# Kernel tuning notes

Hardware: AMD Instinct MI355X
Metric: run time of the kernel (lower is better)

The kernel has to match this reference:

```python
import jax, jax.numpy as jnp
import numpy as np
import math

K = 20        # args.k  (global-branch neighbors)
KL = 20       # args.kl (local-branch neighbors)
EPS = 1e-5    # BatchNorm eps
SLOPE = 0.2   # LeakyReLU slope


def _knn(x, k, keep):
    # x: [B,C,N]; keep: [B,N] bool column mask. pd = -||xi - xj||^2.
    xx = jnp.sum(x * x, axis=1)                          # [B,N]
    inner = jnp.einsum('bci,bcj->bij', x, x)             # [B,N,N]
    pd = 2.0 * inner - xx[:, :, None] - xx[:, None, :]
    mn = jnp.min(pd, axis=-1)                            # per-row min
    # suppressed columns are set to the row min so topk never selects them
    pd = jnp.where(keep[:, None, :], pd, mn[:, :, None])
    return jax.lax.top_k(pd, k)[1]                       # [B,N,k]


def _gather(pts, idx):
    # pts: [B,N,C], idx: [B,N,k] -> [B,N,k,C]
    b = jnp.arange(pts.shape[0])[:, None, None]
    return pts[b, idx]


def _edge_feat(x, k, keep, smooth):
    # DGCNN edge features: concat(neighbor - center, center) -> [B,2C,N,k]
    idx = _knn(x, k, keep)
    xp = jnp.transpose(x, (0, 2, 1))                     # [B,N,C]
    if smooth:
        # GraphLayer: neighbors come from a topk-mean smoothed field
        knn_x = _gather(xp, idx)                         # [B,N,k,C]
        k2 = math.ceil(k * 2 / 3)
        top = jax.lax.top_k(jnp.transpose(knn_x, (0, 1, 3, 2)), k2)[0]
        src = jnp.mean(top, axis=-1)                     # [B,N,C]
    else:
        src = xp
    feat = _gather(src, idx)                             # [B,N,k,C]
    ctr = jnp.broadcast_to(xp[:, :, None, :], feat.shape)
    out = jnp.concatenate([feat - ctr, ctr], axis=-1)    # [B,N,k,2C]
    return jnp.transpose(out, (0, 3, 1, 2))


def _bn(y, axes):
    # BatchNorm (training-mode batch stats, gamma=1, beta=0 as at init)
    mu = jnp.mean(y, axis=axes, keepdims=True)
    var = jnp.var(y, axis=axes, keepdims=True)
    return (y - mu) * jax.lax.rsqrt(var + EPS)


def _conv_block(x, w, axes):
    # 1x1 conv (no bias) + BN + LeakyReLU
    ein = 'oc,bcnk->bonk' if x.ndim == 4 else 'oc,bcn->bon'
    return jax.nn.leaky_relu(_bn(jnp.einsum(ein, w, x), axes), SLOPE)


def _forward(x, local_idx, w1, w2, w3, w4, w5, w6, w7, w8, w9,
             l1w, l2w, l2b, l3w, l3b):
    keep_l = local_idx
    keep_g = jnp.logical_not(local_idx)
    ax4 = (0, 2, 3)
    # local (smoothed GraphLayer) branch, neighbors restricted to local points
    xl1 = _conv_block(_edge_feat(x,   KL, keep_l, True), w1, ax4).max(-1)
    xl2 = _conv_block(_edge_feat(xl1, KL, keep_l, True), w2, ax4).max(-1)
    xl3 = _conv_block(_edge_feat(xl2, KL, keep_l, True), w3, ax4).max(-1)
    xl4 = _conv_block(_edge_feat(xl3, KL, keep_l, True), w4, ax4).max(-1)
    x_local = jnp.concatenate([xl1, xl2, xl3, xl4], axis=1)  # [B,512,N]
    # global branch, neighbors restricted to non-local points
    xg1 = _conv_block(_edge_feat(x,   K, keep_g, False), w5, ax4).max(-1)
    xg2 = _conv_block(_edge_feat(xg1, K, keep_g, False), w6, ax4).max(-1)
    xg3 = _conv_block(_edge_feat(xg2, K, keep_g, False), w7, ax4).max(-1)
    xg4 = _conv_block(_edge_feat(xg3, K, keep_g, False), w8, ax4).max(-1)
    x_glob = jnp.concatenate([xg1, xg2, xg3, xg4], axis=1)   # [B,512,N]
    # per-point merge: local columns take the local-branch features
    h = jnp.where(local_idx[:, None, :], x_local, x_glob)
    h = _conv_block(h, w9, (0, 2))                            # [B,E,N]
    g = jnp.concatenate([h.max(-1), h.mean(-1)], axis=1)      # [B,2E]
    # head: linears + BN1d + LeakyReLU; dropout is identity (eval mode)
    g = jax.nn.leaky_relu(_bn(g @ l1w.T, (0,)), SLOPE)
    g = jax.nn.leaky_relu(_bn(g @ l2w.T + l2b, (0,)), SLOPE)
    return g @ l3w.T + l3b


def setup_inputs() -> dict:
    key = jax.random.key(0)
    ks = jax.random.split(key, 16)
    B, N, E, OUT = 4, 2048, 1024, 40

    def w(k, o, i):
        return jax.random.normal(k, (o, i), jnp.float32) / np.sqrt(i)

    return {
        'x': jax.random.normal(ks[0], (B, 3, N), jnp.float32),
        'local_idx': jax.random.bernoulli(ks[1], 0.5, (B, N)),
        'geod_dist': jax.random.normal(ks[2], (B, N), jnp.float32),
        'w1': w(ks[3], 64, 6),   'w2': w(ks[4], 64, 128),
        'w3': w(ks[5], 128, 128), 'w4': w(ks[6], 256, 256),
        'w5': w(ks[7], 64, 6),   'w6': w(ks[8], 64, 128),
        'w7': w(ks[9], 128, 128), 'w8': w(ks[10], 256, 256),
        'w9': w(ks[11], E, 512),
        'l1w': w(ks[12], 512, 2 * E),
        'l2w': w(ks[13], 256, 512),
        'l2b': jnp.zeros((256,), jnp.float32),
        'l3w': w(ks[14], OUT, 256),
        'l3b': jnp.zeros((OUT,), jnp.float32),
    }


def reference(x, local_idx, geod_dist, w1, w2, w3, w4, w5, w6, w7, w8, w9,
              l1w, l2w, l2b, l3w, l3b):
    del geod_dist  # accepted but unused in the original forward
    return _forward(x, local_idx, w1, w2, w3, w4, w5, w6, w7, w8, w9,
                    l1w, l2w, l2b, l3w, l3b)
```

## Files before the change

kernel.cpp:

```cpp
#include <hip/hip_runtime.h>
#include <hip/hip_bf16.h>
#include <cfloat>

#define BB 4
#define NN 2048
#define KNN 20
#define KTOP 14
#define EPSBN 1e-5f
#define SLOPE 0.2f

__global__ void k_xx3(const float* __restrict__ x, float* __restrict__ xx) {
  int t = blockIdx.x * 64 + threadIdx.x;
  int b = t >> 11, n = t & 2047;
  const float* xb = x + (long)b * (3L * NN) + n;
  float v0 = xb[0], v1 = xb[NN], v2 = xb[2 * NN];
  xx[t] = v0 * v0 + v1 * v1 + v2 * v2;
}

__device__ __forceinline__ void top1_tree(const float v[32], float& bv, int& bi) {
  float mv[16]; int mi[16];
#pragma unroll
  for (int s = 0; s < 16; ++s) {
    mi[s] = (v[2 * s] >= v[2 * s + 1]) ? 2 * s : 2 * s + 1;
    mv[s] = fmaxf(v[2 * s], v[2 * s + 1]);
  }
#pragma unroll
  for (int s = 0; s < 8; ++s) {
    mi[s] = (mv[2 * s] >= mv[2 * s + 1]) ? mi[2 * s] : mi[2 * s + 1];
    mv[s] = fmaxf(mv[2 * s], mv[2 * s + 1]);
  }
#pragma unroll
  for (int s = 0; s < 4; ++s) {
    mi[s] = (mv[2 * s] >= mv[2 * s + 1]) ? mi[2 * s] : mi[2 * s + 1];
    mv[s] = fmaxf(mv[2 * s], mv[2 * s + 1]);
  }
  int i01 = (mv[0] >= mv[1]) ? mi[0] : mi[1];
  float v01 = fmaxf(mv[0], mv[1]);
  int i23 = (mv[2] >= mv[3]) ? mi[2] : mi[3];
  float v23 = fmaxf(mv[2], mv[3]);
  bi = (v01 >= v23) ? i01 : i23;
  bv = fmaxf(v01, v23);
}

__device__ __forceinline__ void remove_slot(float v[32], int bi) {
#pragma unroll
  for (int s = 0; s < 32; ++s)
    if (s == bi) v[s] = -FLT_MAX;
}

__device__ __forceinline__ void sel_reg(const float* __restrict__ trow,
                                        const int* __restrict__ lrow,
                                        int keepv, int lane,
                                        int* __restrict__ orow) {
  int base = 4 * lane;
  float v[32];
#pragma unroll
  for (int q = 0; q < 8; ++q) {
    float4 lv = *(const float4*)(trow + 256 * q + base);
    int4 kv = *(const int4*)(lrow + 256 * q + base);
    v[4 * q + 0] = (((kv.x != 0) ? 1 : 0) == keepv) ? lv.x : -FLT_MAX;
    v[4 * q + 1] = (((kv.y != 0) ? 1 : 0) == keepv) ? lv.y : -FLT_MAX;
    v[4 * q + 2] = (((kv.z != 0) ? 1 : 0) == keepv) ? lv.z : -FLT_MAX;
    v[4 * q + 3] = (((kv.w != 0) ? 1 : 0) == keepv) ? lv.w : -FLT_MAX;
  }
  float bv1, bv2; int li1, li2;
  top1_tree(v, bv1, li1); remove_slot(v, li1);
  top1_tree(v, bv2, li2); remove_slot(v, li2);
  bool has2 = true;
  for (int t = 0; t < KNN; ++t) {
    float gv = bv1;
#pragma unroll
    for (int d = 1; d < 64; d <<= 1) gv = fmaxf(gv, __shfl_xor(gv, d));
    unsigned long long mk = __ballot(bv1 == gv);
    int wl = (int)(__ffsll((long long)mk) - 1);
    int jloc = 256 * (li1 >> 2) + base + (li1 & 3);
    int bj = __shfl(jloc, wl);
    if (lane == 0) orow[t] = bj;
    bool iwin = (lane == wl);
    bool refill = iwin && !has2;
    if (iwin && has2) { bv1 = bv2; li1 = li2; has2 = false; }
    if (__ballot(refill)) {
      if (refill) { top1_tree(v, bv1, li1); remove_slot(v, li1); }
    }
  }
}

template <int C>
__device__ __forceinline__ void pd_tile(
    float (*tile)[NN], float (*a_lds)[4],
    const float* __restrict__ xb, const float* __restrict__ xxb,
    int i0, int tid) {
  for (int jt = 0; jt < NN; jt += 1024) {
    float acc[4][4];
#pragma unroll
    for (int r = 0; r < 4; ++r)
#pragma unroll
      for (int s = 0; s < 4; ++s) acc[r][s] = 0.f;
#pragma unroll 4
    for (int c = 0; c < C; ++c) {
      float4 a = *(const float4*)&a_lds[c][0];
      float4 h = *(const float4*)&xb[(long)c * NN + jt + tid * 4];
      acc[0][0] += a.x * h.x; acc[0][1] += a.x * h.y; acc[0][2] += a.x * h.z; acc[0][3] += a.x * h.w;
      acc[1][0] += a.y * h.x; acc[1][1] += a.y * h.y; acc[1][2] += a.y * h.z; acc[1][3] += a.y * h.w;
      acc[2][0] += a.z * h.x; acc[2][1] += a.z * h.y; acc[2][2] += a.z * h.z; acc[2][3] += a.z * h.w;
      acc[3][0] += a.w * h.x; acc[3][1] += a.w * h.y; acc[3][2] += a.w * h.z; acc[3][3] += a.w * h.w;
    }
    float4 xxj = *(const float4*)&xxb[jt + tid * 4];
#pragma unroll
    for (int r = 0; r < 4; ++r) {
      float xxi = xxb[i0 + r];
      float4 o;
      o.x = 2.f * acc[r][0] - xxi - xxj.x;
      o.y = 2.f * acc[r][1] - xxi - xxj.y;
      o.z = 2.f * acc[r][2] - xxi - xxj.z;
      o.w = 2.f * acc[r][3] - xxi - xxj.w;
      *(float4*)&tile[r][jt + tid * 4] = o;
    }
  }
}

template <int C>
__global__ __launch_bounds__(256) void k_knn_dual(
    const float* __restrict__ xbase, long bstride, const float* __restrict__ xxbase,
    const int* __restrict__ lidx,
    int* __restrict__ idxA , int* __restrict__ idxB ) {
  __shared__ float tile[4][NN];
  __shared__ float a_lds[C][4];
  int b = blockIdx.y;
  int i0 = blockIdx.x * 4;
  const float* xb = xbase + (long)b * bstride;
  const float* xxb = xxbase + b * NN;
  int tid = threadIdx.x, wid = tid >> 6, lane = tid & 63;
  for (int t = tid; t < 4 * C; t += 256) {
    int c = t >> 2, r = t & 3;
    a_lds[c][r] = xb[(long)c * NN + i0 + r];
  }
  __syncthreads();
  pd_tile<C>(tile, a_lds, xb, xxb, i0, tid);
  __syncthreads();
  const int* lrow = lidx + b * NN;
  int i = i0 + wid;
  const float* trow = &tile[wid][0];
  sel_reg(trow, lrow, 1, lane, idxA + ((long)b * NN + i) * KNN);
  sel_reg(trow, lrow, 0, lane, idxB + ((long)b * NN + i) * KNN);
}

template <int C>
__global__ __launch_bounds__(256) void k_knn2(
    const float* __restrict__ xA, const float* __restrict__ xxA,
    int* __restrict__ idxA,
    const float* __restrict__ xB, const float* __restrict__ xxB,
    int* __restrict__ idxB, long bstride, const int* __restrict__ lidx) {
  __shared__ float tile[4][NN];
  __shared__ float a_lds[C][4];
  int half = blockIdx.z;
  const float* xbase = half ? xB : xA;
  const float* xxbase = half ? xxB : xxA;
  int keepv = half ? 0 : 1;
  int* idxO = half ? idxB : idxA;
  int b = blockIdx.y;
  int i0 = blockIdx.x * 4;
  const float* xb = xbase + (long)b * bstride;
  const float* xxb = xxbase + b * NN;
  int tid = threadIdx.x, wid = tid >> 6, lane = tid & 63;
  for (int t = tid; t < 4 * C; t += 256) {
    int c = t >> 2, r = t & 3;
    a_lds[c][r] = xb[(long)c * NN + i0 + r];
  }
  __syncthreads();
  pd_tile<C>(tile, a_lds, xb, xxb, i0, tid);
  __syncthreads();
  const int* lrow = lidx + b * NN;
  int i = i0 + wid;
  sel_reg(&tile[wid][0], lrow, keepv, lane, idxO + ((long)b * NN + i) * KNN);
}

__global__ void k_smooth(const float* __restrict__ x, long bstride, int C,
                         const int* __restrict__ idx, float* __restrict__ src) {
  long t = (long)blockIdx.x * blockDim.x + threadIdx.x;
  if (t >= (long)BB * C * NN) return;
  int n = (int)(t % NN);
  int c = (int)((t / NN) % C);
  int b = (int)(t / ((long)NN * C));
  const int* id = idx + ((long)b * NN + n) * KNN;
  const float* xb = x + (long)b * bstride + (long)c * NN;
  float v[KNN]; float sum = 0.f;
#pragma unroll
  for (int kk = 0; kk < KNN; ++kk) { v[kk] = xb[id[kk]]; sum += v[kk]; }
  int r0 = -1, r1 = -1, r2 = -1, r3 = -1, r4 = -1, r5 = -1;
#pragma unroll
  for (int r = 0; r < KNN - KTOP; ++r) {
    float mvv = FLT_MAX; int mi = -1;
#pragma unroll
    for (int j = 0; j < KNN; ++j) {
      if (j == r0 || j == r1 || j == r2 || j == r3 || j == r4 || j == r5) continue;
      if (v[j] < mvv) { mvv = v[j]; mi = j; }
    }
    sum -= mvv;
    if (r == 0) r0 = mi; else if (r == 1) r1 = mi; else if (r == 2) r2 = mi;
    else if (r == 3) r3 = mi; else if (r == 4) r4 = mi; else r5 = mi;
  }
  src[((long)b * C + c) * NN + n] = sum * (1.f / KTOP);
}

__global__ void k_wprep_all(
    const float* __restrict__ w1, const float* __restrict__ w2,
    const float* __restrict__ w3, const float* __restrict__ w4,
    const float* __restrict__ w5, const float* __restrict__ w6,
    const float* __restrict__ w7, const float* __restrict__ w8,
    float* __restrict__ wa, float* __restrict__ wd) {
  int L = blockIdx.y;
  const float* w; int O, C; long off;
  switch (L) {
    case 0: w = w1; O = 64;  C = 3;   off = 0;     break;
    case 1: w = w2; O = 64;  C = 64;  off = 192;   break;
    case 2: w = w3; O = 128; C = 64;  off = 4288;  break;
    case 3: w = w4; O = 256; C = 128; off = 12480; break;
    case 4: w = w5; O = 64;  C = 3;   off = 45248; break;
    case 5: w = w6; O = 64;  C = 64;  off = 45440; break;
    case 6: w = w7; O = 128; C = 64;  off = 49536; break;
    default: w = w8; O = 256; C = 128; off = 57728; break;
  }
  for (int t = blockIdx.x * blockDim.x + threadIdx.x; t < O * C;
       t += gridDim.x * blockDim.x) {
    int o = t / C, c = t % C;
    float a = w[(long)o * 2 * C + c];
    float bb = w[(long)o * 2 * C + C + c];
    wa[off + (long)c * O + o] = a;
    wd[off + (long)c * O + o] = bb - a;
  }
}

template <int C>
__global__ __launch_bounds__(256) void k_zt2(
    const float* __restrict__ Ma, long mas,
    const float* __restrict__ Mb_, long mbs,
    const float* __restrict__ wa, const float* __restrict__ wd,
    int O, float* __restrict__ Zs, float* __restrict__ Zd) {
  constexpr int KC = (C >= 16) ? 16 : C;
  __shared__ float As[KC][64], Bs[KC][64];
  int z = blockIdx.z;
  int nyo = gridDim.y >> 1;
  int half = (blockIdx.y >= nyo) ? 1 : 0;
  int o0 = (half ? (blockIdx.y - nyo) : blockIdx.y) * 64;
  const float* M = half ? Mb_ : Ma;
  long ms = half ? mbs : mas;
  const float* Wt = half ? wd : wa;
  float* T = half ? Zd : Zs;
  const float* Mb = M + (long)z * ms;
  float* Tb = T + (long)z * NN * O;
  int tid = threadIdx.x;
  int tx = tid & 15, ty = tid >> 4;
  int n0 = blockIdx.x * 64;
  float acc[4][4];
#pragma unroll
  for (int r = 0; r < 4; ++r)
#pragma unroll
    for (int s = 0; s < 4; ++s) acc[r][s] = 0.f;
  for (int c0 = 0; c0 < C; c0 += KC) {
    for (int e = tid; e < KC * 64; e += 256) {
      int c = e >> 6, ii = e & 63;
      As[c][ii] = Mb[(long)(c0 + c) * NN + n0 + ii];
      Bs[c][ii] = Wt[(long)(c0 + c) * O + o0 + ii];
    }
    __syncthreads();
#pragma unroll
    for (int cc = 0; cc < KC; ++cc) {
      float4 a = *(const float4*)&As[cc][ty * 4];
      float4 h = *(const float4*)&Bs[cc][tx * 4];
      acc[0][0] += a.x * h.x; acc[0][1] += a.x * h.y; acc[0][2] += a.x * h.z; acc[0][3] += a.x * h.w;
      acc[1][0] += a.y * h.x; acc[1][1] += a.y * h.y; acc[1][2] += a.y * h.z; acc[1][3] += a.y * h.w;
      acc[2][0] += a.z * h.x; acc[2][1] += a.z * h.y; acc[2][2] += a.z * h.z; acc[2][3] += a.z * h.w;
      acc[3][0] += a.w * h.x; acc[3][1] += a.w * h.y; acc[3][2] += a.w * h.z; acc[3][3] += a.w * h.w;
    }
    __syncthreads();
  }
#pragma unroll
  for (int r = 0; r < 4; ++r) {
    float4 v; v.x = acc[r][0]; v.y = acc[r][1]; v.z = acc[r][2]; v.w = acc[r][3];
    *(float4*)&Tb[(long)(n0 + ty * 4 + r) * O + o0 + tx * 4] = v;
  }
}

template <int O, int PTS>
__global__ __launch_bounds__(O) void k_gmax(
    const float* __restrict__ Zs, const float* __restrict__ Zd,
    const int* __restrict__ idx, float* __restrict__ ymax,
    float* __restrict__ stats) {
  int tid = threadIdx.x;
  int bn0 = blockIdx.x * PTS;
  int b = bn0 >> 11;
  long zbase = (long)b * NN * O;
  float ss = 0.f, sq = 0.f;
  for (int p = 0; p < PTS; ++p) {
    int bn = bn0 + p;
    const int* ir = idx + (long)bn * KNN;
    float zd = Zd[(long)bn * O + tid];
    float smax = -FLT_MAX;
#pragma unroll
    for (int k = 0; k < KNN; ++k) {
      float y = Zs[zbase + (long)ir[k] * O + tid] + zd;
      smax = fmaxf(smax, y); ss += y; sq += y * y;
    }
    ymax[(long)bn * O + tid] = smax;
  }
  atomicAdd(&stats[tid], ss);
  atomicAdd(&stats[O + tid], sq);
}

__global__ void k_bnmax(const float* __restrict__ ymax, const float* __restrict__ stats,
                        int O, float invcnt, float* __restrict__ out, long out_bstride,
                        float* __restrict__ xxout) {
  long t = (long)blockIdx.x * blockDim.x + threadIdx.x;
  if (t >= (long)BB * O * NN) return;
  int n = (int)(t % NN);
  int o = (int)((t / NN) % O);
  int b = (int)(t / ((long)NN * O));
  float mu = stats[o] * invcnt;
  float var = stats[O + o] * invcnt - mu * mu;
  float rs = rsqrtf(var + EPSBN);
  float v = (ymax[((long)b * NN + n) * O + o] - mu) * rs;
  v = v >= 0.f ? v : SLOPE * v;
  out[(long)b * out_bstride + (long)o * NN + n] = v;
  if (xxout) atomicAdd(&xxout[b * NN + n], v * v);
}

__global__ __launch_bounds__(256) void k_gemm9(
    const float* __restrict__ W, const float* __restrict__ xl,
    const float* __restrict__ xg, const int* __restrict__ lidx,
    float* __restrict__ h2, float* __restrict__ stats) {
  __shared__ float Ws[16][72];
  __shared__ float Hs[16][132];
  int tid = threadIdx.x;
  int tx = tid & 31, ty = tid >> 5;
  int p0 = blockIdx.x * 128, o0 = blockIdx.y * 64;
  int b = p0 >> 11, n0 = p0 & 2047;
  int sp = tid & 127, scq = (tid >> 7) * 8;
  const float* hbase;
  {
    int pt = p0 + sp;
    hbase = (lidx[pt] ? xl : xg) + (long)b * (512L * NN) + (pt & 2047);
  }
  int wo = tid >> 2, wc = (tid & 3) * 4;
  float acc[8][4];
#pragma unroll
  for (int i = 0; i < 8; ++i)
#pragma unroll
    for (int j = 0; j < 4; ++j) acc[i][j] = 0.f;

  for (int c0 = 0; c0 < 512; c0 += 16) {
    float4 wv = *(const float4*)(W + (long)(o0 + wo) * 512 + c0 + wc);
    Ws[wc + 0][wo] = wv.x; Ws[wc + 1][wo] = wv.y;
    Ws[wc + 2][wo] = wv.z; Ws[wc + 3][wo] = wv.w;
    long crow = (long)(c0 + scq) * NN;
#pragma unroll
    for (int e = 0; e < 8; ++e) Hs[scq + e][sp] = hbase[crow + (long)e * NN];
    __syncthreads();
#pragma unroll
    for (int cc = 0; cc < 16; ++cc) {
      float4 a0 = *(const float4*)&Ws[cc][ty * 8];
      float4 a1 = *(const float4*)&Ws[cc][ty * 8 + 4];
      float4 h = *(const float4*)&Hs[cc][tx * 4];
      acc[0][0] += a0.x * h.x; acc[0][1] += a0.x * h.y; acc[0][2] += a0.x * h.z; acc[0][3] += a0.x * h.w;
      acc[1][0] += a0.y * h.x; acc[1][1] += a0.y * h.y; acc[1][2] += a0.y * h.z; acc[1][3] += a0.y * h.w;
      acc[2][0] += a0.z * h.x; acc[2][1] += a0.z * h.y; acc[2][2] += a0.z * h.z; acc[2][3] += a0.z * h.w;
      acc[3][0] += a0.w * h.x; acc[3][1] += a0.w * h.y; acc[3][2] += a0.w * h.z; acc[3][3] += a0.w * h.w;
      acc[4][0] += a1.x * h.x; acc[4][1] += a1.x * h.y; acc[4][2] += a1.x * h.z; acc[4][3] += a1.x * h.w;
      acc[5][0] += a1.y * h.x; acc[5][1] += a1.y * h.y; acc[5][2] += a1.y * h.z; acc[5][3] += a1.y * h.w;
      acc[6][0] += a1.z * h.x; acc[6][1] += a1.z * h.y; acc[6][2] += a1.z * h.z; acc[6][3] += a1.z * h.w;
      acc[7][0] += a1.w * h.x; acc[7][1] += a1.w * h.y; acc[7][2] += a1.w * h.z; acc[7][3] += a1.w * h.w;
    }
    __syncthreads();
  }
#pragma unroll
  for (int i = 0; i < 8; ++i) {
    int o = o0 + ty * 8 + i;
    float4 v; v.x = acc[i][0]; v.y = acc[i][1]; v.z = acc[i][2]; v.w = acc[i][3];
    *(float4*)&h2[((long)b * 1024 + o) * NN + n0 + tx * 4] = v;
    float ss = acc[i][0] + acc[i][1] + acc[i][2] + acc[i][3];
    float sq = acc[i][0] * acc[i][0] + acc[i][1] * acc[i][1] +
               acc[i][2] * acc[i][2] + acc[i][3] * acc[i][3];
    for (int d = 16; d > 0; d >>= 1) {
      ss += __shfl_down(ss, d, 32);
      sq += __shfl_down(sq, d, 32);
    }
    if (tx == 0) {
      atomicAdd(&stats[o], ss);
      atomicAdd(&stats[1024 + o], sq);
    }
  }
}

__global__ void k_gpool(const float* __restrict__ h2, const float* __restrict__ stats,
                        float* __restrict__ g) {
  int b = blockIdx.x / 1024, o = blockIdx.x % 1024;
  int tid = threadIdx.x;
  float mu = stats[o] * (1.f / 8192.f);
  float var = stats[1024 + o] * (1.f / 8192.f) - mu * mu;
  float rs = rsqrtf(var + EPSBN);
  const float* hr = h2 + ((long)b * 1024 + o) * NN;
  float mx = -FLT_MAX, sm = 0.f;
  for (int n = tid; n < NN; n += 256) {
    float v = (hr[n] - mu) * rs; v = v >= 0.f ? v : SLOPE * v;
    mx = fmaxf(mx, v); sm += v;
  }
  __shared__ float smx[256], ssm[256];
  smx[tid] = mx; ssm[tid] = sm; __syncthreads();
  for (int s = 128; s > 0; s >>= 1) {
    if (tid < s) { smx[tid] = fmaxf(smx[tid], smx[tid + s]); ssm[tid] += ssm[tid + s]; }
    __syncthreads();
  }
  if (tid == 0) { g[b * 2048 + o] = smx[0]; g[b * 2048 + 1024 + o] = ssm[0] * (1.f / NN); }
}

__global__ void k_head(const float* __restrict__ gin, int CIN, const float* __restrict__ wl,
                       const float* __restrict__ bias, float* __restrict__ gout, int do_bn) {
  int f = blockIdx.x, tid = threadIdx.x, F = gridDim.x;
  const float* wr = wl + (long)f * CIN;
  float a0 = 0, a1 = 0, a2 = 0, a3 = 0;
  for (int c = tid; c < CIN; c += 256) {
    float wv = wr[c];
    a0 += wv * gin[c];         a1 += wv * gin[CIN + c];
    a2 += wv * gin[2 * CIN + c]; a3 += wv * gin[3 * CIN + c];
  }
  __shared__ float s0[256], s1[256], s2[256], s3[256];
  s0[tid] = a0; s1[tid] = a1; s2[tid] = a2; s3[tid] = a3; __syncthreads();
  for (int s = 128; s > 0; s >>= 1) {
    if (tid < s) { s0[tid] += s0[tid + s]; s1[tid] += s1[tid + s];
                   s2[tid] += s2[tid + s]; s3[tid] += s3[tid + s]; }
    __syncthreads();
  }
  if (tid == 0) {
    float z0 = s0[0], z1 = s1[0], z2 = s2[0], z3 = s3[0];
    if (bias) { float bb = bias[f]; z0 += bb; z1 += bb; z2 += bb; z3 += bb; }
    if (do_bn) {
      float mu = 0.25f * (z0 + z1 + z2 + z3);
      float var = 0.25f * (z0 * z0 + z1 * z1 + z2 * z2 + z3 * z3) - mu * mu;
      float rs = rsqrtf(var + EPSBN);
      z0 = (z0 - mu) * rs; z1 = (z1 - mu) * rs; z2 = (z2 - mu) * rs; z3 = (z3 - mu) * rs;
      z0 = z0 >= 0.f ? z0 : SLOPE * z0; z1 = z1 >= 0.f ? z1 : SLOPE * z1;
      z2 = z2 >= 0.f ? z2 : SLOPE * z2; z3 = z3 >= 0.f ? z3 : SLOPE * z3;
    }
    gout[0 * F + f] = z0; gout[1 * F + f] = z1; gout[2 * F + f] = z2; gout[3 * F + f] = z3;
  }
}

extern "C" void kernel_launch(void* const* d_in, const int* in_sizes, int n_in,
                              void* d_out, int out_size, void* d_ws, size_t ws_size,
                              hipStream_t stream) {
  const float* x   = (const float*)d_in[0];
  const int*   lidx= (const int*)d_in[1];
  const float* w1  = (const float*)d_in[3];
  const float* w2  = (const float*)d_in[4];
  const float* w3  = (const float*)d_in[5];
  const float* w4  = (const float*)d_in[6];
  const float* w5  = (const float*)d_in[7];
  const float* w6  = (const float*)d_in[8];
  const float* w7  = (const float*)d_in[9];
  const float* w8  = (const float*)d_in[10];
  const float* w9  = (const float*)d_in[11];
  const float* l1w = (const float*)d_in[12];
  const float* l2w = (const float*)d_in[13];
  const float* l2b = (const float*)d_in[14];
  const float* l3w = (const float*)d_in[15];
  const float* l3b = (const float*)d_in[16];
  float* out = (float*)d_out;

  float* ws    = (float*)d_ws;
  float* xxall = ws;
  float* stats = ws + 57344;
  int*   idxb  = (int*)(ws + 61440);
  float* xloc  = ws + 225280;
  float* xglb  = ws + 4419584;
  float* big   = ws + 8613888;
  float* g     = ws + 17002496;
  float* g1    = ws + 17010688;
  float* g2    = ws + 17012736;
  float* waall = ws + 17013760;
  float* wdall = ws + 17104256;

  float* srcb  = big;
  float* Zs    = big + 1048576;
  float* Zd    = big + 3145728;
  float* ymaxb = big + 5242880;
  int*   idxG2 = (int*)(big + 7340032);
  float* h2    = big;
  int*   idxG  = (int*)xglb;

  float* xxS0 = xxall;
  float* xxS1 = xxall + 8192;
  float* xxS2 = xxall + 16384;
  float* xxS3 = xxall + 24576;
  float* xxS4 = xxall + 32768;
  float* xxS5 = xxall + 40960;
  float* xxS6 = xxall + 49152;

  float* SL1 = stats + 0;    float* SL2 = stats + 128;
  float* SL3 = stats + 256;  float* SL4 = stats + 512;
  float* SG1 = stats + 1024; float* SG2 = stats + 1152;
  float* SG3 = stats + 1280; float* SG4 = stats + 1536;
  float* S9  = stats + 2048;

  const float invE = 1.f / (BB * NN * KNN);
  const long XS0 = 3L * NN;
  const long XS  = 512L * NN;
  const dim3 gknn(NN / 4, BB);
  const dim3 gknn2(NN / 4, BB, 2);

  hipMemsetAsync(ws, 0, 61440 * sizeof(float), stream);
  k_wprep_all<<<dim3(128, 8), 256, 0, stream>>>(w1, w2, w3, w4, w5, w6, w7, w8,
                                                waall, wdall);
  k_xx3<<<128, 64, 0, stream>>>(x, xxS0);

  k_knn_dual<3><<<gknn, 256, 0, stream>>>(x, XS0, xxS0, lidx, idxb, idxG);

  k_smooth<<<(BB * 3 * NN + 255) / 256, 256, 0, stream>>>(x, XS0, 3, idxb, srcb);
  k_zt2<3><<<dim3(32, 2, 4), 256, 0, stream>>>(srcb, 3L * NN, x, XS0,
                                               waall + 0, wdall + 0, 64, Zs, Zd);
  k_gmax<64, 8><<<BB * NN / 8, 64, 0, stream>>>(Zs, Zd, idxb, ymaxb, SL1);
  k_bnmax<<<(BB * 64 * NN + 255) / 256, 256, 0, stream>>>(ymaxb, SL1, 64, invE,
                                                          xloc + 0 * NN, XS, xxS1);
  k_zt2<3><<<dim3(32, 2, 4), 256, 0, stream>>>(x, XS0, x, XS0,
                                               waall + 45248, wdall + 45248, 64, Zs, Zd);
  k_gmax<64, 8><<<BB * NN / 8, 64, 0, stream>>>(Zs, Zd, idxG, ymaxb, SG1);
  k_bnmax<<<(BB * 64 * NN + 255) / 256, 256, 0, stream>>>(ymaxb, SG1, 64, invE,
                                                          xglb + 0 * NN, XS, xxS4);

  k_knn2<64><<<gknn2, 256, 0, stream>>>(xloc, xxS1, idxb,
                                        xglb, xxS4, idxG2, XS, lidx);
  k_smooth<<<(BB * 64 * NN + 255) / 256, 256, 0, stream>>>(xloc, XS, 64, idxb, srcb);
  k_zt2<64><<<dim3(32, 2, 4), 256, 0, stream>>>(srcb, 64L * NN, xloc, XS,
                                                waall + 192, wdall + 192, 64, Zs, Zd);
  k_gmax<64, 8><<<BB * NN / 8, 64, 0, stream>>>(Zs, Zd, idxb, ymaxb, SL2);
  k_bnmax<<<(BB * 64 * NN + 255) / 256, 256, 0, stream>>>(ymaxb, SL2, 64, invE,
                                                          xloc + 64 * NN, XS, xxS2);
  k_zt2<64><<<dim3(32, 2, 4), 256, 0, stream>>>(xglb, XS, xglb, XS,
                                                waall + 45440, wdall + 45440, 64, Zs, Zd);
  k_gmax<64, 8><<<BB * NN / 8, 64, 0, stream>>>(Zs, Zd, idxG2, ymaxb, SG2);
  k_bnmax<<<(BB * 64 * NN + 255) / 256, 256, 0, stream>>>(ymaxb, SG2, 64, invE,
                                                          xglb + 64 * NN, XS, xxS5);

  k_knn2<64><<<gknn2, 256, 0, stream>>>(xloc + 64 * NN, xxS2, idxb,
                                        xglb + 64 * NN, xxS5, idxG2, XS, lidx);
  k_smooth<<<(BB * 64 * NN + 255) / 256, 256, 0, stream>>>(xloc + 64 * NN, XS, 64, idxb, srcb);
  k_zt2<64><<<dim3(32, 4, 4), 256, 0, stream>>>(srcb, 64L * NN, xloc + 64 * NN, XS,
                                                waall + 4288, wdall + 4288, 128, Zs, Zd);
  k_gmax<128, 16><<<BB * NN / 16, 128, 0, stream>>>(Zs, Zd, idxb, ymaxb, SL3);
  k_bnmax<<<(BB * 128 * NN + 255) / 256, 256, 0, stream>>>(ymaxb, SL3, 128, invE,
                                                           xloc + 128 * NN, XS, xxS3);
  k_zt2<64><<<dim3(32, 4, 4), 256, 0, stream>>>(xglb + 64 * NN, XS, xglb + 64 * NN, XS,
                                                waall + 49536, wdall + 49536, 128, Zs, Zd);
  k_gmax<128, 16><<<BB * NN / 16, 128, 0, stream>>>(Zs, Zd, idxG2, ymaxb, SG3);
  k_bnmax<<<(BB * 128 * NN + 255) / 256, 256, 0, stream>>>(ymaxb, SG3, 128, invE,
                                                           xglb + 128 * NN, XS, xxS6);

  k_knn2<128><<<gknn2, 256, 0, stream>>>(xloc + 128 * NN, xxS3, idxb,
                                         xglb + 128 * NN, xxS6, idxG2, XS, lidx);
  k_smooth<<<(BB * 128 * NN + 255) / 256, 256, 0, stream>>>(xloc + 128 * NN, XS, 128, idxb, srcb);
  k_zt2<128><<<dim3(32, 8, 4), 256, 0, stream>>>(srcb, 128L * NN, xloc + 128 * NN, XS,
                                                 waall + 12480, wdall + 12480, 256, Zs, Zd);
  k_gmax<256, 16><<<BB * NN / 16, 256, 0, stream>>>(Zs, Zd, idxb, ymaxb, SL4);
  k_bnmax<<<(BB * 256 * NN + 255) / 256, 256, 0, stream>>>(ymaxb, SL4, 256, invE,
                                                           xloc + 256 * NN, XS, nullptr);
  k_zt2<128><<<dim3(32, 8, 4), 256, 0, stream>>>(xglb + 128 * NN, XS, xglb + 128 * NN, XS,
                                                 waall + 57728, wdall + 57728, 256, Zs, Zd);
  k_gmax<256, 16><<<BB * NN / 16, 256, 0, stream>>>(Zs, Zd, idxG2, ymaxb, SG4);
  k_bnmax<<<(BB * 256 * NN + 255) / 256, 256, 0, stream>>>(ymaxb, SG4, 256, invE,
                                                           xglb + 256 * NN, XS, nullptr);

  {
    dim3 g9(NN * BB / 128, 1024 / 64);
    k_gemm9<<<g9, 256, 0, stream>>>(w9, xloc, xglb, lidx, h2, S9);
  }
  k_gpool<<<BB * 1024, 256, 0, stream>>>(h2, S9, g);
  k_head<<<512, 256, 0, stream>>>(g, 2048, l1w, nullptr, g1, 1);
  k_head<<<256, 256, 0, stream>>>(g1, 512, l2w, l2b, g2, 1);
  k_head<<<40, 256, 0, stream>>>(g2, 256, l3w, l3b, out, 0);
}
```

Measured before the change: 1.391 ms.

## Cache kNN candidate values in LDS tile instead of registers during selection

The top-k selection no longer keeps its 32-value candidate array live in registers. It writes the masked values back into the shared distance tile and rereads them from LDS only when a lane needs a refill, with removal done by a single LDS store. The a_lds staging buffer is dropped and the centre-point features are read straight from global memory. Because the tile is now overwritten, the dual kernel recomputes the distance tile for its second mask pass. The aim is to cut register pressure and raise occupancy, at the cost of extra LDS traffic, a second distance computation, and uncoalesced global reads of the centre points.

Measured after the change: 1.255 ms. -9.8%, faster.

```diff
diff --git a/kernel.cpp b/kernel.cpp
--- a/kernel.cpp
+++ b/kernel.cpp
@@ -42,30 +42,39 @@
   bv = fmaxf(v01, v23);
 }
 
-__device__ __forceinline__ void remove_slot(float v[32], int bi) {
-#pragma unroll
-  for (int s = 0; s < 32; ++s)
-    if (s == bi) v[s] = -FLT_MAX;
-}
-
-__device__ __forceinline__ void sel_reg(const float* __restrict__ trow,
-                                        const int* __restrict__ lrow,
-                                        int keepv, int lane,
-                                        int* __restrict__ orow) {
+__device__ __forceinline__ void sel_cached(float* __restrict__ trow,
+                                           const int* __restrict__ lrow,
+                                           int keepv, int lane,
+                                           int* __restrict__ orow) {
   int base = 4 * lane;
-  float v[32];
-#pragma unroll
-  for (int q = 0; q < 8; ++q) {
-    float4 lv = *(const float4*)(trow + 256 * q + base);
-    int4 kv = *(const int4*)(lrow + 256 * q + base);
-    v[4 * q + 0] = (((kv.x != 0) ? 1 : 0) == keepv) ? lv.x : -FLT_MAX;
-    v[4 * q + 1] = (((kv.y != 0) ? 1 : 0) == keepv) ? lv.y : -FLT_MAX;
-    v[4 * q + 2] = (((kv.z != 0) ? 1 : 0) == keepv) ? lv.z : -FLT_MAX;
-    v[4 * q + 3] = (((kv.w != 0) ? 1 : 0) == keepv) ? lv.w : -FLT_MAX;
-  }
   float bv1, bv2; int li1, li2;
-  top1_tree(v, bv1, li1); remove_slot(v, li1);
-  top1_tree(v, bv2, li2); remove_slot(v, li2);
+  {
+    float v[32];
+#pragma unroll
+    for (int q = 0; q < 8; ++q) {
+      float4 lv = *(const float4*)(trow + 256 * q + base);
+      int4 kv = *(const int4*)(lrow + 256 * q + base);
+      v[4 * q + 0] = (((kv.x != 0) ? 1 : 0) == keepv) ? lv.x : -FLT_MAX;
+      v[4 * q + 1] = (((kv.y != 0) ? 1 : 0) == keepv) ? lv.y : -FLT_MAX;
+      v[4 * q + 2] = (((kv.z != 0) ? 1 : 0) == keepv) ? lv.z : -FLT_MAX;
+      v[4 * q + 3] = (((kv.w != 0) ? 1 : 0) == keepv) ? lv.w : -FLT_MAX;
+    }
+    top1_tree(v, bv1, li1);
+#pragma unroll
+    for (int s = 0; s < 32; ++s)
+      if (s == li1) v[s] = -FLT_MAX;
+    top1_tree(v, bv2, li2);
+#pragma unroll
+    for (int s = 0; s < 32; ++s)
+      if (s == li2) v[s] = -FLT_MAX;
+#pragma unroll
+    for (int q = 0; q < 8; ++q) {
+      float4 sv;
+      sv.x = v[4 * q + 0]; sv.y = v[4 * q + 1];
+      sv.z = v[4 * q + 2]; sv.w = v[4 * q + 3];
+      *(float4*)(trow + 256 * q + base) = sv;
+    }
+  }
   bool has2 = true;
   for (int t = 0; t < KNN; ++t) {
     float gv = bv1;
@@ -77,17 +86,27 @@
     int bj = __shfl(jloc, wl);
     if (lane == 0) orow[t] = bj;
     bool iwin = (lane == wl);
-    bool refill = iwin && !has2;
+    bool needref = iwin && !has2;
     if (iwin && has2) { bv1 = bv2; li1 = li2; has2 = false; }
-    if (__ballot(refill)) {
-      if (refill) { top1_tree(v, bv1, li1); remove_slot(v, li1); }
+    if (__ballot(needref)) {
+      if (needref) {
+        float w[32];
+#pragma unroll
+        for (int q = 0; q < 8; ++q) {
+          float4 lv = *(const float4*)(trow + 256 * q + base);
+          w[4 * q + 0] = lv.x; w[4 * q + 1] = lv.y;
+          w[4 * q + 2] = lv.z; w[4 * q + 3] = lv.w;
+        }
+        top1_tree(w, bv1, li1);
+        trow[256 * (li1 >> 2) + base + (li1 & 3)] = -FLT_MAX;
+      }
     }
   }
 }
 
 template <int C>
 __device__ __forceinline__ void pd_tile(
-    float (*tile)[NN], float (*a_lds)[4],
+    float (*tile)[NN],
     const float* __restrict__ xb, const float* __restrict__ xxb,
     int i0, int tid) {
   for (int jt = 0; jt < NN; jt += 1024) {
@@ -98,7 +117,7 @@
       for (int s = 0; s < 4; ++s) acc[r][s] = 0.f;
 #pragma unroll 4
     for (int c = 0; c < C; ++c) {
-      float4 a = *(const float4*)&a_lds[c][0];
+      float4 a = *(const float4*)&xb[(long)c * NN + i0];
       float4 h = *(const float4*)&xb[(long)c * NN + jt + tid * 4];
       acc[0][0] += a.x * h.x; acc[0][1] += a.x * h.y; acc[0][2] += a.x * h.z; acc[0][3] += a.x * h.w;
       acc[1][0] += a.y * h.x; acc[1][1] += a.y * h.y; acc[1][2] += a.y * h.z; acc[1][3] += a.y * h.w;
@@ -125,24 +144,22 @@
     const int* __restrict__ lidx,
     int* __restrict__ idxA , int* __restrict__ idxB ) {
   __shared__ float tile[4][NN];
-  __shared__ float a_lds[C][4];
   int b = blockIdx.y;
   int i0 = blockIdx.x * 4;
   const float* xb = xbase + (long)b * bstride;
   const float* xxb = xxbase + b * NN;
   int tid = threadIdx.x, wid = tid >> 6, lane = tid & 63;
-  for (int t = tid; t < 4 * C; t += 256) {
-    int c = t >> 2, r = t & 3;
-    a_lds[c][r] = xb[(long)c * NN + i0 + r];
-  }
-  __syncthreads();
-  pd_tile<C>(tile, a_lds, xb, xxb, i0, tid);
-  __syncthreads();
   const int* lrow = lidx + b * NN;
   int i = i0 + wid;
-  const float* trow = &tile[wid][0];
-  sel_reg(trow, lrow, 1, lane, idxA + ((long)b * NN + i) * KNN);
-  sel_reg(trow, lrow, 0, lane, idxB + ((long)b * NN + i) * KNN);
+  for (int pass = 0; pass < 2; ++pass) {
+    if (pass) __syncthreads();
+    pd_tile<C>(tile, xb, xxb, i0, tid);
+    __syncthreads();
+    float* trow = &tile[wid][0];
+    int kvp = pass ? 0 : 1;
+    int* ob = pass ? idxB : idxA;
+    sel_cached(trow, lrow, kvp, lane, ob + ((long)b * NN + i) * KNN);
+  }
 }
 
 template <int C>
@@ -152,7 +169,6 @@
     const float* __restrict__ xB, const float* __restrict__ xxB,
     int* __restrict__ idxB, long bstride, const int* __restrict__ lidx) {
   __shared__ float tile[4][NN];
-  __shared__ float a_lds[C][4];
   int half = blockIdx.z;
   const float* xbase = half ? xB : xA;
   const float* xxbase = half ? xxB : xxA;
@@ -163,16 +179,11 @@
   const float* xb = xbase + (long)b * bstride;
   const float* xxb = xxbase + b * NN;
   int tid = threadIdx.x, wid = tid >> 6, lane = tid & 63;
-  for (int t = tid; t < 4 * C; t += 256) {
-    int c = t >> 2, r = t & 3;
-    a_lds[c][r] = xb[(long)c * NN + i0 + r];
-  }
-  __syncthreads();
-  pd_tile<C>(tile, a_lds, xb, xxb, i0, tid);
+  pd_tile<C>(tile, xb, xxb, i0, tid);
   __syncthreads();
   const int* lrow = lidx + b * NN;
   int i = i0 + wid;
-  sel_reg(&tile[wid][0], lrow, keepv, lane, idxO + ((long)b * NN + i) * KNN);
+  sel_cached(&tile[wid][0], lrow, keepv, lane, idxO + ((long)b * NN + i) * KNN);
 }
 
 __global__ void k_smooth(const float* __restrict__ x, long bstride, int C,
```
